# Optimization experiments

Hardware: AMD Instinct MI355X
Metric: run time of the kernel (lower is better)

## Reference

```python
import jax, jax.numpy as jnp
import numpy as np

VOCAB = 82
EMBED = 256
HIDDEN = 128
PAD = 0


def setup_inputs() -> dict:
    key = jax.random.key(0)
    ks = jax.random.split(key, 7)
    B, T = 256, 512
    sqrt_k = (1.0 / HIDDEN) ** 0.5
    tokens = jax.random.randint(ks[0], (B, T), 0, VOCAB)
    emb = jax.random.normal(ks[1], (VOCAB, EMBED), dtype=jnp.float32)
    emb = emb.at[PAD].set(0.0)  # padding_idx row is zero
    W_f = jax.random.uniform(ks[2], (HIDDEN, HIDDEN + EMBED), minval=-sqrt_k, maxval=sqrt_k)
    W_c = jax.random.uniform(ks[3], (HIDDEN, HIDDEN + EMBED), minval=-sqrt_k, maxval=sqrt_k)
    W_o = jax.random.uniform(ks[4], (HIDDEN, HIDDEN + EMBED), minval=-sqrt_k, maxval=sqrt_k)
    clf_W = jax.random.uniform(ks[5], (VOCAB, HIDDEN), minval=-sqrt_k, maxval=sqrt_k)
    clf_b = jax.random.uniform(ks[6], (VOCAB,), minval=-sqrt_k, maxval=sqrt_k)
    return {"batch_reviews": tokens, "emb": emb, "W_f": W_f, "W_c": W_c,
            "W_o": W_o, "clf_W": clf_W, "clf_b": clf_b}


def reference(batch_reviews, emb, W_f, W_c, W_o, clf_W, clf_b):
    # embed: [B, T, E]
    data = emb[batch_reviews]
    B, T, E = data.shape
    # scan over time: carry = (h, c); emit gate signals per step
    xs = jnp.swapaxes(data, 0, 1)  # [T, B, E]

    def step(carry, x_t):
        h, c = carry
        hx = jnp.concatenate([h, x_t], axis=1)            # [B, H+E]
        f = jax.nn.sigmoid(hx @ W_f.T)                    # [B, H]
        o = jax.nn.sigmoid(hx @ W_o.T)
        c_tilde = jnp.tanh(hx @ W_c.T)
        next_c = f * c + (1.0 - f) * c_tilde              # coupled forget/input gate
        next_h = o * jnp.tanh(next_c)
        return (next_h, next_c), (f, o, c_tilde)

    h0 = jnp.zeros((B, HIDDEN), dtype=data.dtype)
    c0 = jnp.zeros((B, HIDDEN), dtype=data.dtype)
    (h_T, c_T), (f_all, o_all, ct_all) = jax.lax.scan(step, (h0, c0), xs)
    logits = h_T @ clf_W.T + clf_b                        # [B, VOCAB]
    # gate stacks are [T, B, H], matching torch's per-step list of gate tuples
    return logits, f_all, o_all, ct_all
```

## Files before the change

kernel.cpp:

```cpp
#include <hip/hip_runtime.h>

#define VOCAB  82
#define EMBED  256
#define HIDDEN 128
#define BATCH  256
#define SEQ    512
#define KX     (HIDDEN + EMBED)
#define SEG    36

__device__ __align__(16) float Gv_buf[VOCAB * 3 * HIDDEN];

__device__ __forceinline__ float fast_sigmoid(float x) {
    return 1.f / (1.f + __expf(-x));
}
__device__ __forceinline__ float fast_tanh(float x) {
    x = fminf(fmaxf(x, -15.f), 15.f);
    float e = __expf(2.f * x);
    return (e - 1.f) / (e + 1.f);
}
__device__ __forceinline__ float quad_sum(float x) {
    int y1 = __builtin_amdgcn_mov_dpp(__float_as_int(x), 0xB1, 0xF, 0xF, true);
    x = x + __int_as_float(y1);
    int y2 = __builtin_amdgcn_mov_dpp(__float_as_int(x), 0x4E, 0xF, 0xF, true);
    return x + __int_as_float(y2);
}

__global__ __launch_bounds__(128, 2)
void gv_prologue(const float* __restrict__ emb,
                 const float* __restrict__ Wf,
                 const float* __restrict__ Wc,
                 const float* __restrict__ Wo) {
    const int g = blockIdx.x % 3;
    const int v = blockIdx.x / 3;
    const int r = threadIdx.x;

    __shared__ __align__(16) float e_lds[EMBED];
    e_lds[r]       = emb[(size_t)v * EMBED + r];
    e_lds[r + 128] = emb[(size_t)v * EMBED + r + 128];
    __syncthreads();

    const float* Wg = (g == 0) ? Wf : (g == 1) ? Wo : Wc;
    const float4* wr = (const float4*)(Wg + (size_t)r * KX + HIDDEN);
    const float4* ev = (const float4*)e_lds;
    float a0 = 0.f, a1 = 0.f, a2 = 0.f, a3 = 0.f;
#pragma unroll
    for (int i = 0; i < EMBED / 4; ++i) {
        float4 w4 = wr[i];
        float4 e4 = ev[i];
        a0 += w4.x * e4.x;
        a1 += w4.y * e4.y;
        a2 += w4.z * e4.z;
        a3 += w4.w * e4.w;
    }
    Gv_buf[(size_t)v * 384 + g * 128 + r] = (a0 + a1) + (a2 + a3);
}

__global__ __launch_bounds__(512, 2)
void lstm_main(const int* __restrict__ tokens,
               const float* __restrict__ Wf,
               const float* __restrict__ Wc,
               const float* __restrict__ Wo,
               const float* __restrict__ clfW,
               const float* __restrict__ clfb,
               float* __restrict__ out) {
    const int b   = blockIdx.x;
    const int tid = threadIdx.x;
    const int q   = tid & 3;
    const int r   = tid >> 2;

    __shared__ __align__(16) float hbuf[2][4 * SEG];
    __shared__ int tok[SEQ];

    float4 wf[8], wo[8], wc[8];
    {
        const float4* pf = (const float4*)(Wf + (size_t)r * KX + q * 32);
        const float4* po = (const float4*)(Wo + (size_t)r * KX + q * 32);
        const float4* pc = (const float4*)(Wc + (size_t)r * KX + q * 32);
#pragma unroll
        for (int i = 0; i < 8; ++i) { wf[i] = pf[i]; wo[i] = po[i]; wc[i] = pc[i]; }
    }

    tok[tid] = tokens[(size_t)b * SEQ + tid];
    if (tid < HIDDEN) hbuf[0][(tid >> 5) * SEG + (tid & 31)] = 0.f;
    float c = 0.f;
    __syncthreads();

    const size_t GATE0 = (size_t)BATCH * VOCAB;
    const size_t GSZ   = (size_t)SEQ * BATCH * HIDDEN;
    float* gout = out + GATE0 + (size_t)q * GSZ + (size_t)b * HIDDEN + r;

    for (int t = 0; t < SEQ; ++t) {
        const int p  = t & 1;
        const int tk = tok[t];
        const float gx = (q < 3) ? Gv_buf[tk * 384 + q * 128 + r] : 0.f;

        const float4* hv4 = (const float4*)&hbuf[p][q * SEG];
        float pf = 0.f, po = 0.f, pc = 0.f;
#pragma unroll
        for (int i = 0; i < 8; ++i) {
            float4 h4 = hv4[i];
            pf += wf[i].x * h4.x; pf += wf[i].y * h4.y;
            pf += wf[i].z * h4.z; pf += wf[i].w * h4.w;
            po += wo[i].x * h4.x; po += wo[i].y * h4.y;
            po += wo[i].z * h4.z; po += wo[i].w * h4.w;
            pc += wc[i].x * h4.x; pc += wc[i].y * h4.y;
            pc += wc[i].z * h4.z; pc += wc[i].w * h4.w;
        }
        pf += (q == 0) ? gx : 0.f;
        po += (q == 1) ? gx : 0.f;
        pc += (q == 2) ? gx : 0.f;

        const float pre_f = quad_sum(pf);
        const float pre_o = quad_sum(po);
        const float pre_c = quad_sum(pc);

        const float f  = fast_sigmoid(pre_f);
        const float o  = fast_sigmoid(pre_o);
        const float ct = fast_tanh(pre_c);
        c = f * c + (1.f - f) * ct;
        const float h = o * fast_tanh(c);

        if (q == 0) hbuf[1 - p][(r >> 5) * SEG + (r & 31)] = h;
        __syncthreads();
        const float sval = (q == 0) ? f : (q == 1) ? o : ct;
        if (q < 3) gout[(size_t)t * (BATCH * HIDDEN)] = sval;
    }

    if (tid < 4 * VOCAB) {
        const int v = tid >> 2;
        const float4* cw  = (const float4*)(clfW + (size_t)v * HIDDEN + q * 32);
        const float4* hv4 = (const float4*)&hbuf[0][q * SEG];
        float a = 0.f;
#pragma unroll
        for (int i = 0; i < 8; ++i) {
            float4 w4 = cw[i];
            float4 h4 = hv4[i];
            a += w4.x * h4.x + w4.y * h4.y + w4.z * h4.z + w4.w * h4.w;
        }
        a = quad_sum(a);
        if (q == 0) out[(size_t)b * VOCAB + v] = a + clfb[v];
    }
}

extern "C" void kernel_launch(void* const* d_in, const int* in_sizes, int n_in,
                              void* d_out, int out_size, void* d_ws, size_t ws_size,
                              hipStream_t stream) {
    const int*   tokens = (const int*)  d_in[0];
    const float* emb    = (const float*)d_in[1];
    const float* Wf     = (const float*)d_in[2];
    const float* Wc     = (const float*)d_in[3];
    const float* Wo     = (const float*)d_in[4];
    const float* clfW   = (const float*)d_in[5];
    const float* clfb   = (const float*)d_in[6];
    float*       out    = (float*)d_out;

    gv_prologue<<<3 * VOCAB, 128, 0, stream>>>(emb, Wf, Wc, Wo);
    lstm_main<<<BATCH, 512, 0, stream>>>(tokens, Wf, Wc, Wo, clfW, clfb, out);
}
```

Baseline: 563.3 us.

## Split hidden dot products across eight lanes with 1024-thread blocks and raw exp/rcp

Doubles threads per batch block from 512 to 1024, so each hidden unit's three gate dot products are split across eight lanes of 16 elements instead of four lanes of 32. The partial sums are reduced with an added ds_swizzle step. This shortens each thread's serial FMA chain per time step, which is the sequential critical path. The change also uses raw v_exp_f32/v_rcp_f32 for sigmoid and tanh, drops the tanh clamp, and replaces __syncthreads with an explicit lgkmcnt wait plus barrier. In exchange it pays a larger barrier cost and an extra cross-lane reduction step, and the unclamped tanh may lose accuracy at extreme inputs.

```diff
diff --git a/kernel.cpp b/kernel.cpp
--- a/kernel.cpp
+++ b/kernel.cpp
@@ -6,23 +6,51 @@
 #define BATCH  256
 #define SEQ    512
 #define KX     (HIDDEN + EMBED)
-#define SEG    36
+#define HPAD   20
 
 __device__ __align__(16) float Gv_buf[VOCAB * 3 * HIDDEN];
 
+__device__ __forceinline__ float vrcp(float x)  { float r; asm("v_rcp_f32 %0, %1" : "=v"(r) : "v"(x)); return r; }
+__device__ __forceinline__ float vexp2(float x) { float r; asm("v_exp_f32 %0, %1" : "=v"(r) : "v"(x)); return r; }
+#define LOG2E 1.4426950408889634f
+
 __device__ __forceinline__ float fast_sigmoid(float x) {
-    return 1.f / (1.f + __expf(-x));
+    return vrcp(1.f + vexp2(-LOG2E * x));
 }
 __device__ __forceinline__ float fast_tanh(float x) {
-    x = fminf(fmaxf(x, -15.f), 15.f);
-    float e = __expf(2.f * x);
-    return (e - 1.f) / (e + 1.f);
+    return fmaf(-2.f, vrcp(1.f + vexp2((2.f * LOG2E) * x)), 1.f);
 }
-__device__ __forceinline__ float quad_sum(float x) {
+
+__device__ __forceinline__ float oct_sum(float x) {
     int y1 = __builtin_amdgcn_mov_dpp(__float_as_int(x), 0xB1, 0xF, 0xF, true);
-    x = x + __int_as_float(y1);
+    x += __int_as_float(y1);
     int y2 = __builtin_amdgcn_mov_dpp(__float_as_int(x), 0x4E, 0xF, 0xF, true);
-    return x + __int_as_float(y2);
+    x += __int_as_float(y2);
+    int y3 = __builtin_amdgcn_ds_swizzle(__float_as_int(x), 0x101F);
+    x += __int_as_float(y3);
+    return x;
+}
+
+#define PIN(x)  asm volatile("" : "+v"(x))
+#define PIN4(v) do { PIN(v.x); PIN(v.y); PIN(v.z); PIN(v.w); } while (0)
+
+__device__ __forceinline__ void block_sync_lds() {
+    asm volatile("s_waitcnt lgkmcnt(0)" ::: "memory");
+    __builtin_amdgcn_s_barrier();
+    __builtin_amdgcn_sched_barrier(0);
+}
+
+__device__ __forceinline__ float dot16(float4 a0, float4 a1, float4 a2, float4 a3,
+                                       float4 h0, float4 h1, float4 h2, float4 h3) {
+    float s = a0.x * h0.x;
+    s = fmaf(a0.y, h0.y, s); s = fmaf(a0.z, h0.z, s); s = fmaf(a0.w, h0.w, s);
+    s = fmaf(a1.x, h1.x, s); s = fmaf(a1.y, h1.y, s); s = fmaf(a1.z, h1.z, s);
+    s = fmaf(a1.w, h1.w, s);
+    s = fmaf(a2.x, h2.x, s); s = fmaf(a2.y, h2.y, s); s = fmaf(a2.z, h2.z, s);
+    s = fmaf(a2.w, h2.w, s);
+    s = fmaf(a3.x, h3.x, s); s = fmaf(a3.y, h3.y, s); s = fmaf(a3.z, h3.z, s);
+    s = fmaf(a3.w, h3.w, s);
+    return s;
 }
 
 __global__ __launch_bounds__(128, 2)
@@ -55,89 +83,81 @@
     Gv_buf[(size_t)v * 384 + g * 128 + r] = (a0 + a1) + (a2 + a3);
 }
 
-__global__ __launch_bounds__(512, 2)
-void lstm_main(const int* __restrict__ tokens,
-               const float* __restrict__ Wf,
-               const float* __restrict__ Wc,
-               const float* __restrict__ Wo,
-               const float* __restrict__ clfW,
-               const float* __restrict__ clfb,
-               float* __restrict__ out) {
+__global__ void __attribute__((amdgpu_flat_work_group_size(1024, 1024),
+                               amdgpu_waves_per_eu(4, 4)))
+lstm_main(const int* __restrict__ tokens,
+          const float* __restrict__ Wf,
+          const float* __restrict__ Wc,
+          const float* __restrict__ Wo,
+          const float* __restrict__ clfW,
+          const float* __restrict__ clfb,
+          float* __restrict__ out) {
     const int b   = blockIdx.x;
     const int tid = threadIdx.x;
-    const int q   = tid & 3;
-    const int r   = tid >> 2;
+    const int q   = tid & 7;
+    const int r   = tid >> 3;
 
-    __shared__ __align__(16) float hbuf[2][4 * SEG];
+    __shared__ __align__(16) float hbuf[2][8 * HPAD];
     __shared__ int tok[SEQ];
 
-    float4 wf[8], wo[8], wc[8];
-    {
-        const float4* pf = (const float4*)(Wf + (size_t)r * KX + q * 32);
-        const float4* po = (const float4*)(Wo + (size_t)r * KX + q * 32);
-        const float4* pc = (const float4*)(Wc + (size_t)r * KX + q * 32);
-#pragma unroll
-        for (int i = 0; i < 8; ++i) { wf[i] = pf[i]; wo[i] = po[i]; wc[i] = pc[i]; }
-    }
+    const float4* PF = (const float4*)(Wf + (size_t)r * KX + q * 16);
+    const float4* PO = (const float4*)(Wo + (size_t)r * KX + q * 16);
+    const float4* PC = (const float4*)(Wc + (size_t)r * KX + q * 16);
+    float4 F0 = PF[0], F1 = PF[1], F2 = PF[2], F3 = PF[3];
+    float4 O0 = PO[0], O1 = PO[1], O2 = PO[2], O3 = PO[3];
+    float4 C0 = PC[0], C1 = PC[1], C2 = PC[2], C3 = PC[3];
+    PIN4(F0); PIN4(F1); PIN4(F2); PIN4(F3);
+    PIN4(O0); PIN4(O1); PIN4(O2); PIN4(O3);
+    PIN4(C0); PIN4(C1); PIN4(C2); PIN4(C3);
 
-    tok[tid] = tokens[(size_t)b * SEQ + tid];
-    if (tid < HIDDEN) hbuf[0][(tid >> 5) * SEG + (tid & 31)] = 0.f;
+    if (tid < SEQ)    tok[tid] = tokens[(size_t)b * SEQ + tid];
+    if (tid < HIDDEN) hbuf[0][(tid >> 4) * HPAD + (tid & 15)] = 0.f;
     float c = 0.f;
     __syncthreads();
 
-    const size_t GATE0 = (size_t)BATCH * VOCAB;
-    const size_t GSZ   = (size_t)SEQ * BATCH * HIDDEN;
-    float* gout = out + GATE0 + (size_t)q * GSZ + (size_t)b * HIDDEN + r;
+    const size_t GSZ = (size_t)SEQ * BATCH * HIDDEN;
+    float* gout = out + (size_t)BATCH * VOCAB
+                      + (size_t)(q < 3 ? q : 0) * GSZ
+                      + (size_t)b * HIDDEN + r;
 
     for (int t = 0; t < SEQ; ++t) {
         const int p  = t & 1;
         const int tk = tok[t];
-        const float gx = (q < 3) ? Gv_buf[tk * 384 + q * 128 + r] : 0.f;
+        float gx = 0.f;
+        if (q < 3) gx = Gv_buf[tk * 384 + q * 128 + r];
 
-        const float4* hv4 = (const float4*)&hbuf[p][q * SEG];
-        float pf = 0.f, po = 0.f, pc = 0.f;
-#pragma unroll
-        for (int i = 0; i < 8; ++i) {
-            float4 h4 = hv4[i];
-            pf += wf[i].x * h4.x; pf += wf[i].y * h4.y;
-            pf += wf[i].z * h4.z; pf += wf[i].w * h4.w;
-            po += wo[i].x * h4.x; po += wo[i].y * h4.y;
-            po += wo[i].z * h4.z; po += wo[i].w * h4.w;
-            pc += wc[i].x * h4.x; pc += wc[i].y * h4.y;
-            pc += wc[i].z * h4.z; pc += wc[i].w * h4.w;
-        }
+        const float4* hv = (const float4*)&hbuf[p][q * HPAD];
+        float4 h0 = hv[0], h1 = hv[1], h2 = hv[2], h3 = hv[3];
+
+        float pf = dot16(F0, F1, F2, F3, h0, h1, h2, h3);
+        float po = dot16(O0, O1, O2, O3, h0, h1, h2, h3);
+        float pc = dot16(C0, C1, C2, C3, h0, h1, h2, h3);
         pf += (q == 0) ? gx : 0.f;
         po += (q == 1) ? gx : 0.f;
         pc += (q == 2) ? gx : 0.f;
 
-        const float pre_f = quad_sum(pf);
-        const float pre_o = quad_sum(po);
-        const float pre_c = quad_sum(pc);
+        pf = oct_sum(pf);
+        po = oct_sum(po);
+        pc = oct_sum(pc);
 
-        const float f  = fast_sigmoid(pre_f);
-        const float o  = fast_sigmoid(pre_o);
-        const float ct = fast_tanh(pre_c);
-        c = f * c + (1.f - f) * ct;
+        const float f  = fast_sigmoid(pf);
+        const float o  = fast_sigmoid(po);
+        const float ct = fast_tanh(pc);
+        c = fmaf(f, c - ct, ct);
         const float h = o * fast_tanh(c);
 
-        if (q == 0) hbuf[1 - p][(r >> 5) * SEG + (r & 31)] = h;
-        __syncthreads();
+        if (q == 0) hbuf[1 - p][(r >> 4) * HPAD + (r & 15)] = h;
+        block_sync_lds();
         const float sval = (q == 0) ? f : (q == 1) ? o : ct;
         if (q < 3) gout[(size_t)t * (BATCH * HIDDEN)] = sval;
     }
 
-    if (tid < 4 * VOCAB) {
-        const int v = tid >> 2;
-        const float4* cw  = (const float4*)(clfW + (size_t)v * HIDDEN + q * 32);
-        const float4* hv4 = (const float4*)&hbuf[0][q * SEG];
-        float a = 0.f;
-#pragma unroll
-        for (int i = 0; i < 8; ++i) {
-            float4 w4 = cw[i];
-            float4 h4 = hv4[i];
-            a += w4.x * h4.x + w4.y * h4.y + w4.z * h4.z + w4.w * h4.w;
-        }
-        a = quad_sum(a);
+    if (tid < 8 * VOCAB) {
+        const int v = tid >> 3;
+        const float4* cw = (const float4*)(clfW + (size_t)v * HIDDEN + q * 16);
+        const float4* hp = (const float4*)&hbuf[0][q * HPAD];
+        float a = dot16(cw[0], cw[1], cw[2], cw[3], hp[0], hp[1], hp[2], hp[3]);
+        a = oct_sum(a);
         if (q == 0) out[(size_t)b * VOCAB + v] = a + clfb[v];
     }
 }
@@ -155,5 +175,5 @@
     float*       out    = (float*)d_out;
 
     gv_prologue<<<3 * VOCAB, 128, 0, stream>>>(emb, Wf, Wc, Wo);
-    lstm_main<<<BATCH, 512, 0, stream>>>(tokens, Wf, Wc, Wo, clfW, clfb, out);
+    lstm_main<<<BATCH, 1024, 0, stream>>>(tokens, Wf, Wc, Wo, clfW, clfb, out);
 }
```

After: 554.8 us. No clear change (-1.5%).
